# Kernel optimization log

Hardware: AMD Instinct MI355X
Metric: run time of the kernel (lower is better)

## Reference

```python
import jax, jax.numpy as jnp
import numpy as np
from jax import lax


@jax.custom_vjp
def binarize(w):
    # sign binarization of weights (XNOR-style), STE gradient in bwd
    return jnp.sign(w)

def _bin_fwd(w):
    return jnp.sign(w), w

def _bin_bwd(w, g):
    # straight-through estimator, clipped to |w| <= 1
    return (g * (jnp.abs(w) <= 1.0).astype(g.dtype),)

binarize.defvjp(_bin_fwd, _bin_bwd)


def hardtanh(x):
    return jnp.clip(x, -1.0, 1.0)


def bconv(x, w, b):
    # x: NCHW, w: OIHW, valid padding, stride 1, binarized weights
    y = lax.conv_general_dilated(
        x, binarize(w), window_strides=(1, 1), padding='VALID',
        dimension_numbers=('NCHW', 'OIHW', 'NCHW'))
    return y + b[None, :, None, None]


def maxpool2(x):
    return lax.reduce_window(x, -jnp.inf, lax.max,
                             window_dimensions=(1, 1, 2, 2),
                             window_strides=(1, 1, 2, 2),
                             padding='VALID')


def setup_inputs() -> dict:
    key = jax.random.key(0)
    ks = jax.random.split(key, 11)
    f32 = jnp.float32
    sc = 0.1  # keep weights inside the STE clip region mostly
    return {
        'x':  jax.random.normal(ks[0], (2048, 3, 32, 32), f32),
        'w1': jax.random.normal(ks[1], (100, 3, 5, 5), f32) * sc,
        'b1': jax.random.normal(ks[2], (100,), f32) * sc,
        'w2': jax.random.normal(ks[3], (16, 100, 5, 5), f32) * sc,
        'b2': jax.random.normal(ks[4], (16,), f32) * sc,
        'w3': jax.random.normal(ks[5], (120, 400), f32) * sc,
        'b3': jax.random.normal(ks[6], (120,), f32) * sc,
        'w4': jax.random.normal(ks[7], (84, 120), f32) * sc,
        'b4': jax.random.normal(ks[8], (84,), f32) * sc,
        'w5': jax.random.normal(ks[9], (10, 84), f32) * sc,
        'b5': jax.random.normal(ks[10], (10,), f32) * sc,
    }


def reference(x, w1, b1, w2, b2, w3, b3, w4, b4, w5, b5):
    h = maxpool2(hardtanh(bconv(x, w1, b1)))          # [B,100,14,14]
    h = maxpool2(hardtanh(bconv(h, w2, b2)))          # [B,16,5,5]
    h = h.reshape(h.shape[0], 16 * 5 * 5)             # [B,400]
    h = hardtanh(h @ binarize(w3).T + b3)             # [B,120]
    h = hardtanh(h @ binarize(w4).T + b4)             # [B,84]
    return h @ binarize(w5).T + b5                    # [B,10]
```

## Files before the change

kernel.cpp:

```cpp
#include <hip/hip_runtime.h>
#include <hip/hip_bf16.h>
#include <hip/hip_fp16.h>

typedef _Float16 f16x8 __attribute__((ext_vector_type(8)));
typedef float f32x4 __attribute__((ext_vector_type(4)));

union B8 { uint4 u; f16x8 h; };

__device__ __forceinline__ float htanh(float v) {
    return fminf(1.f, fmaxf(-1.f, v));
}
__device__ __forceinline__ unsigned short f2h(float f) {
    __half h = __float2half(f);
    return *reinterpret_cast<unsigned short*>(&h);
}
__device__ __forceinline__ float sxor(float h, float w) {
    return __uint_as_float(__float_as_uint(h) ^ (__float_as_uint(w) & 0x80000000u));
}

#define WSA1_OFF 102400
#define H2_OFF   138240

__global__ __launch_bounds__(256) void bn_pack(
    const float* __restrict__ w1, uint4* __restrict__ wsA1,
    const float* __restrict__ w2, uint4* __restrict__ wsA2)
{
    if (blockIdx.x < 9) {
        int t = blockIdx.x * 256 + threadIdx.x;
        if (t >= 2240) return;
        int lane = t & 63;
        int kk = (t >> 6) % 5;
        int m  = t / 320;
        int oc = m * 16 + (lane & 15), g = lane >> 4;
        unsigned int d[4];
        #pragma unroll
        for (int r = 0; r < 4; ++r) {
            int c, ky, kx; bool tv;
            if (kk < 4) { int rr = kk * 4 + g; tv = rr < 15; c = rr % 3; ky = rr / 3; kx = r; }
            else        { int s  = g * 4 + r;  tv = s  < 15; c = s  % 3; ky = s  / 3; kx = 4; }
            unsigned int v = 0u;
            if (tv && oc < 100) {
                float wv = w1[((oc * 3 + c) * 5 + ky) * 5 + kx];
                unsigned int sg = wv > 0.f ? 0x3C00u : (wv < 0.f ? 0xBC00u : 0u);
                v = sg | (sg << 16);
            }
            d[r] = v;
        }
        wsA1[t] = make_uint4(d[0], d[1], d[2], d[3]);
    } else {
        int t = (blockIdx.x - 9) * 256 + threadIdx.x;
        int lane = t & 63;
        int kk = (t >> 6) & 3;
        int s = t >> 8;
        int oc = lane & 15, g = lane >> 4;
        unsigned int d[4];
        #pragma unroll
        for (int r = 0; r < 4; ++r) {
            unsigned int u[2];
            #pragma unroll
            for (int h = 0; h < 2; ++h) {
                int ic = kk * 32 + g * 8 + r * 2 + h;
                unsigned int v = 0u;
                if (ic < 100) {
                    float wv = w2[(oc * 100 + ic) * 25 + s];
                    v = wv > 0.f ? 0x3C00u : (wv < 0.f ? 0xBC00u : 0u);
                }
                u[h] = v;
            }
            d[r] = u[0] | (u[1] << 16);
        }
        wsA2[t] = make_uint4(d[0], d[1], d[2], d[3]);
    }
}

#define HT_HALVES 29952

template<int MC>
__device__ __forceinline__ void conv1_group(
    const unsigned int* __restrict__ sxu, const uint4* __restrict__ wsA1,
    const float* b1s, unsigned short* ht, int lane, int g, int col,
    int ntStart, int mBase)
{
    f16x8 a[MC][5];
    #pragma unroll
    for (int mi = 0; mi < MC; ++mi)
        #pragma unroll
        for (int kk = 0; kk < 5; ++kk) {
            B8 t; t.u = wsA1[((mBase + mi) * 5 + kk) * 64 + lane];
            a[mi][kk] = t.h;
        }

    const int g37 = g * 37, g148 = g * 148 + 4;

    for (int nt = ntStart; nt < 13; nt += 4) {
        const int w = nt * 16 + col;
        const bool valid = w < 196;
        const int wc = valid ? w : 195;
        const int wy = wc / 14, wx = wc - wy * 14;
        const unsigned int* bt = sxu + wy * 222 + wx * 2;
        const unsigned int* b0  = bt + g37;
        const unsigned int* blx = bt + g148;

        f32x4 mx[MC];
        #pragma unroll
        for (int pass = 0; pass < 4; ++pass) {
            const int q = (pass >> 1) * 111 + (pass & 1);

            f32x4 acc[MC];
            #pragma unroll
            for (int kk = 0; kk < 5; ++kk) {
                B8 bb;
                if (kk < 4) {
                    const unsigned int* bk = b0 + kk * 148;
                    bb.u = make_uint4(bk[q], bk[q + 1], bk[q + 2], bk[q + 3]);
                } else {
                    bb.u = make_uint4(blx[q], blx[q + 37], blx[q + 74], blx[q + 111]);
                }
                #pragma unroll
                for (int mi = 0; mi < MC; ++mi) {
                    f32x4 c0 = (kk == 0) ? (f32x4){0.f, 0.f, 0.f, 0.f} : acc[mi];
                    acc[mi] = __builtin_amdgcn_mfma_f32_16x16x32_f16(a[mi][kk], bb.h, c0, 0, 0, 0);
                }
            }
            #pragma unroll
            for (int mi = 0; mi < MC; ++mi) {
                if (pass == 0) {
                    mx[mi] = acc[mi];
                } else {
                    #pragma unroll
                    for (int r = 0; r < 4; ++r)
                        mx[mi][r] = fmaxf(mx[mi][r], acc[mi][r]);
                }
            }
        }

        if (valid) {
            const int sig = wy * 18 + wx;
            #pragma unroll
            for (int mi = 0; mi < MC; ++mi) {
                const int oc0 = (mBase + mi) * 16 + g * 4;
                if (oc0 < 104) {
                    float4 bias = *(const float4*)&b1s[oc0];
                    unsigned short o0 = f2h(htanh(mx[mi][0] + bias.x));
                    unsigned short o1 = f2h(htanh(mx[mi][1] + bias.y));
                    unsigned short o2 = f2h(htanh(mx[mi][2] + bias.z));
                    unsigned short o3 = f2h(htanh(mx[mi][3] + bias.w));
                    uint2 d;
                    d.x = (unsigned int)o0 | ((unsigned int)o1 << 16);
                    d.y = (unsigned int)o2 | ((unsigned int)o3 << 16);
                    *(uint2*)(ht + sig * 120 + oc0) = d;
                }
            }
        }
    }
}

__global__ __launch_bounds__(256, 2) void bn_convs(
    const float* __restrict__ x, const uint4* __restrict__ wsA1,
    const unsigned short* __restrict__ wsA2,
    const float* __restrict__ b1, const float* __restrict__ b2,
    float* __restrict__ h2)
{
    __shared__ __align__(16) unsigned int sxu[3584];
    __shared__ __align__(16) unsigned short ht[HT_HALVES];
    __shared__ float b1s[112];
    const int img = blockIdx.x;
    const int tid = threadIdx.x;
    const int lane = tid & 63, wv = tid >> 6;

    {
        uint4* z = (uint4*)sxu;
        for (int i = tid; i < 896; i += 256) z[i] = make_uint4(0u, 0u, 0u, 0u);
        uint4* zh = (uint4*)ht;
        for (int i = tid; i < 3744; i += 256) zh[i] = make_uint4(0u, 0u, 0u, 0u);
    }
    __syncthreads();

    {
        const float4* xg = (const float4*)(x + (size_t)img * 3072);
        for (int i = tid; i < 768; i += 256) {
            float4 v = xg[i];
            float vv[4] = {v.x, v.y, v.z, v.w};
            unsigned int u[4];
            #pragma unroll
            for (int q = 0; q < 4; ++q) {
                __half h = __float2half(vv[q]);
                float rs = vv[q] - __half2float(h);
                __half rl = __float2half(rs);
                u[q] = (unsigned int)*(unsigned short*)&h |
                       ((unsigned int)*(unsigned short*)&rl << 16);
            }
            int c = i >> 8, y = (i >> 3) & 31, q4 = i & 7;
            int base = 111 * y + 37 * c + 4 * q4;
            sxu[base]     = u[0];
            sxu[base + 1] = u[1];
            sxu[base + 2] = u[2];
            sxu[base + 3] = u[3];
        }
        if (tid < 112) b1s[tid] = (tid < 100) ? b1[tid] : 0.f;
    }
    __syncthreads();

    const int g = lane >> 4;
    const int col = lane & 15;

    const int s0 = (wv + (img & 3)) & 3;
    conv1_group<4>(sxu, wsA1, b1s, ht, lane, g, col, s0, 0);
    conv1_group<3>(sxu, wsA1, b1s, ht, lane, g, col, s0, 4);
    __syncthreads();

    int bc[7];
    #pragma unroll
    for (int t = 0; t < 7; ++t) {
        int P = t * 16 + col;
        int Pc = P < 100 ? P : 99;
        bc[t] = ((Pc / 10) * 18 + (Pc % 10)) * 120 + g * 8;
    }
    f32x4 acc[7];
    #pragma unroll
    for (int t = 0; t < 7; ++t) acc[t] = (f32x4){0.f, 0.f, 0.f, 0.f};

    const f16x8* wsAv = (const f16x8*)wsA2;
    const int ko = wv * 32;
    {
        f16x8 a2[13];
        #pragma unroll
        for (int j = 0; j < 13; ++j)
            a2[j] = wsAv[((j * 4 + wv) << 6) | lane];
        #pragma unroll
        for (int s = 0; s < 13; ++s) {
            const int off = ((s / 5) * 18 + (s % 5)) * 120 + ko;
            #pragma unroll
            for (int t = 0; t < 7; ++t) {
                f16x8 bb = *(const f16x8*)&ht[bc[t] + off];
                acc[t] = __builtin_amdgcn_mfma_f32_16x16x32_f16(a2[s], bb, acc[t], 0, 0, 0);
            }
        }
    }
    {
        f16x8 a2[12];
        #pragma unroll
        for (int j = 0; j < 12; ++j)
            a2[j] = wsAv[(((13 + j) * 4 + wv) << 6) | lane];
        #pragma unroll
        for (int s = 13; s < 25; ++s) {
            const int off = ((s / 5) * 18 + (s % 5)) * 120 + ko;
            #pragma unroll
            for (int t = 0; t < 7; ++t) {
                f16x8 bb = *(const f16x8*)&ht[bc[t] + off];
                acc[t] = __builtin_amdgcn_mfma_f32_16x16x32_f16(a2[s - 13], bb, acc[t], 0, 0, 0);
            }
        }
    }
    __syncthreads();

    float* pc = (float*)ht;
    #pragma unroll
    for (int t = 0; t < 7; ++t)
        #pragma unroll
        for (int r = 0; r < 4; ++r)
            pc[(((wv * 7 + t) * 16) + (g * 4 + r)) * 16 + col] = acc[t][r];
    __syncthreads();

    float* y = (float*)ht + 7168;
    for (int i = tid; i < 1792; i += 256) {
        int t = i >> 8, rem = i & 255;
        int oc = rem >> 4, c2 = rem & 15;
        int P = t * 16 + c2;
        if (P < 100) {
            int idx = (t * 16 + oc) * 16 + c2;
            float v = pc[idx] + pc[1792 + idx] + pc[3584 + idx] + pc[5376 + idx];
            y[oc * 100 + P] = htanh(v + b2[oc]);
        }
    }
    __syncthreads();

    for (int t2 = tid; t2 < 400; t2 += 256) {
        int oc = t2 / 25, pp = t2 - oc * 25;
        int ppy = pp / 5, ppx = pp - ppy * 5;
        int base = oc * 100 + ppy * 20 + ppx * 2;
        float m = fmaxf(fmaxf(y[base], y[base + 1]),
                        fmaxf(y[base + 10], y[base + 11]));
        h2[(size_t)img * 400 + t2] = m;
    }
}

__global__ __launch_bounds__(256) void bn_fc(
    const float* __restrict__ h2,
    const float* __restrict__ w3, const float* __restrict__ b3,
    const float* __restrict__ w4, const float* __restrict__ b4,
    const float* __restrict__ w5, const float* __restrict__ b5,
    float* __restrict__ out)
{
    __shared__ float sh2[2 * 404];
    __shared__ float sh3[2 * 124];
    __shared__ float sh4[2 * 88];
    const int b0 = blockIdx.x * 2;
    const int tid = threadIdx.x;

    for (int i = tid; i < 800; i += 256) {
        int s = i / 400, k = i - s * 400;
        sh2[s * 404 + k] = h2[(size_t)(b0 + s) * 400 + k];
    }
    __syncthreads();

    for (int t = tid; t < 240; t += 256) {
        int o = t >> 1, s = t & 1;
        const float4* wr = (const float4*)(w3 + o * 400);
        const float4* hr = (const float4*)&sh2[s * 404];
        float a0 = 0.f, a1 = 0.f, a2 = 0.f, a3 = 0.f;
        #pragma unroll 5
        for (int k = 0; k < 100; ++k) {
            float4 w = wr[k], h = hr[k];
            a0 += sxor(h.x, w.x); a1 += sxor(h.y, w.y);
            a2 += sxor(h.z, w.z); a3 += sxor(h.w, w.w);
        }
        sh3[s * 124 + o] = htanh(b3[o] + ((a0 + a1) + (a2 + a3)));
    }
    __syncthreads();

    for (int t = tid; t < 168; t += 256) {
        int o = t >> 1, s = t & 1;
        const float4* wr = (const float4*)(w4 + o * 120);
        const float4* hr = (const float4*)&sh3[s * 124];
        float a0 = 0.f, a1 = 0.f, a2 = 0.f, a3 = 0.f;
        #pragma unroll
        for (int k = 0; k < 30; ++k) {
            float4 w = wr[k], h = hr[k];
            a0 += sxor(h.x, w.x); a1 += sxor(h.y, w.y);
            a2 += sxor(h.z, w.z); a3 += sxor(h.w, w.w);
        }
        sh4[s * 88 + o] = htanh(b4[o] + ((a0 + a1) + (a2 + a3)));
    }
    __syncthreads();

    for (int t = tid; t < 20; t += 256) {
        int o = t >> 1, s = t & 1;
        const float4* wr = (const float4*)(w5 + o * 84);
        const float4* hr = (const float4*)&sh4[s * 88];
        float a0 = 0.f, a1 = 0.f, a2 = 0.f, a3 = 0.f;
        #pragma unroll
        for (int k = 0; k < 21; ++k) {
            float4 w = wr[k], h = hr[k];
            a0 += sxor(h.x, w.x); a1 += sxor(h.y, w.y);
            a2 += sxor(h.z, w.z); a3 += sxor(h.w, w.w);
        }
        out[(size_t)(b0 + s) * 10 + o] = b5[o] + ((a0 + a1) + (a2 + a3));
    }
}

extern "C" void kernel_launch(void* const* d_in, const int* in_sizes, int n_in,
                              void* d_out, int out_size, void* d_ws, size_t ws_size,
                              hipStream_t stream) {
    const float* x  = (const float*)d_in[0];
    const float* w1 = (const float*)d_in[1];
    const float* b1 = (const float*)d_in[2];
    const float* w2 = (const float*)d_in[3];
    const float* b2 = (const float*)d_in[4];
    const float* w3 = (const float*)d_in[5];
    const float* b3 = (const float*)d_in[6];
    const float* w4 = (const float*)d_in[7];
    const float* b4 = (const float*)d_in[8];
    const float* w5 = (const float*)d_in[9];
    const float* b5 = (const float*)d_in[10];
    float* out = (float*)d_out;

    unsigned short* wsA2 = (unsigned short*)d_ws;
    uint4* wsA1          = (uint4*)((char*)d_ws + WSA1_OFF);
    float* h2            = (float*)((char*)d_ws + H2_OFF);

    hipLaunchKernelGGL(bn_pack, dim3(34), dim3(256), 0, stream,
                       w1, wsA1, w2, (uint4*)wsA2);
    hipLaunchKernelGGL(bn_convs, dim3(2048), dim3(256), 0, stream,
                       x, wsA1, wsA2, b1, b2, h2);
    hipLaunchKernelGGL(bn_fc, dim3(1024), dim3(256), 0, stream, h2,
                       w3, b3, w4, b4, w5, b5, out);
}
```

Baseline: 111.1 us.

## Split each image's conv stack across two blocks by output rows

The fused conv kernel now launches two blocks per image, each covering a band of output rows. Each block stages only the input rows it needs, computes the overlapping conv1 rows (a halo), and produces a subset of the pooled conv2 outputs. It also shrinks the conv1 activation tile stride from 120 to 104 halves and fuses the conv2 reduction, bias, hardtanh and maxpool into a single pass. The smaller LDS footprint is meant to raise occupancy and spread work over more blocks, at the cost of recomputing the halo conv1 rows and a dynamic inner MFMA loop that is no longer fully unrolled.

```diff
diff --git a/kernel.cpp b/kernel.cpp
--- a/kernel.cpp
+++ b/kernel.cpp
@@ -73,13 +73,14 @@
     }
 }
 
-#define HT_HALVES 29952
+#define HT_HALVES 18432
+#define SXU_WORDS 2816
 
 template<int MC>
 __device__ __forceinline__ void conv1_group(
     const unsigned int* __restrict__ sxu, const uint4* __restrict__ wsA1,
     const float* b1s, unsigned short* ht, int lane, int g, int col,
-    int ntStart, int mBase)
+    int ntStart, int mBase, int ntiles, int nwin)
 {
     f16x8 a[MC][5];
     #pragma unroll
@@ -92,11 +93,11 @@
 
     const int g37 = g * 37, g148 = g * 148 + 4;
 
-    for (int nt = ntStart; nt < 13; nt += 4) {
-        const int w = nt * 16 + col;
-        const bool valid = w < 196;
-        const int wc = valid ? w : 195;
-        const int wy = wc / 14, wx = wc - wy * 14;
+    for (int nt = ntStart; nt < ntiles; nt += 4) {
+        const int lw = nt * 16 + col;
+        const bool valid = lw < nwin;
+        const int lwc = valid ? lw : nwin - 1;
+        const int wy = lwc / 14, wx = lwc - wy * 14;
         const unsigned int* bt = sxu + wy * 222 + wx * 2;
         const unsigned int* b0  = bt + g37;
         const unsigned int* blx = bt + g148;
@@ -148,7 +149,7 @@
                     uint2 d;
                     d.x = (unsigned int)o0 | ((unsigned int)o1 << 16);
                     d.y = (unsigned int)o2 | ((unsigned int)o3 << 16);
-                    *(uint2*)(ht + sig * 120 + oc0) = d;
+                    *(uint2*)(ht + sig * 104 + oc0) = d;
                 }
             }
         }
@@ -161,25 +162,30 @@
     const float* __restrict__ b1, const float* __restrict__ b2,
     float* __restrict__ h2)
 {
-    __shared__ __align__(16) unsigned int sxu[3584];
+    __shared__ __align__(16) unsigned int sxu[SXU_WORDS];
     __shared__ __align__(16) unsigned short ht[HT_HALVES];
     __shared__ float b1s[112];
-    const int img = blockIdx.x;
+    const int img  = blockIdx.x >> 1;
+    const int half = blockIdx.x & 1;
     const int tid = threadIdx.x;
     const int lane = tid & 63, wv = tid >> 6;
 
     {
         uint4* z = (uint4*)sxu;
-        for (int i = tid; i < 896; i += 256) z[i] = make_uint4(0u, 0u, 0u, 0u);
+        for (int i = tid; i < 704; i += 256) z[i] = make_uint4(0u, 0u, 0u, 0u);
         uint4* zh = (uint4*)ht;
-        for (int i = tid; i < 3744; i += 256) zh[i] = make_uint4(0u, 0u, 0u, 0u);
+        for (int i = tid; i < 2304; i += 256) zh[i] = make_uint4(0u, 0u, 0u, 0u);
     }
     __syncthreads();
 
     {
+        const int ybase = half ? 12 : 0;
+        const int nrows = half ? 20 : 24;
         const float4* xg = (const float4*)(x + (size_t)img * 3072);
-        for (int i = tid; i < 768; i += 256) {
-            float4 v = xg[i];
+        for (int i = tid; i < nrows * 24; i += 256) {
+            int yl = i / 24, rem = i - yl * 24;
+            int c = rem >> 3, q4 = rem & 7;
+            float4 v = xg[c * 256 + (yl + ybase) * 8 + q4];
             float vv[4] = {v.x, v.y, v.z, v.w};
             unsigned int u[4];
             #pragma unroll
@@ -190,8 +196,7 @@
                 u[q] = (unsigned int)*(unsigned short*)&h |
                        ((unsigned int)*(unsigned short*)&rl << 16);
             }
-            int c = i >> 8, y = (i >> 3) & 31, q4 = i & 7;
-            int base = 111 * y + 37 * c + 4 * q4;
+            int base = 111 * yl + 37 * c + 4 * q4;
             sxu[base]     = u[0];
             sxu[base + 1] = u[1];
             sxu[base + 2] = u[2];
@@ -204,21 +209,25 @@
     const int g = lane >> 4;
     const int col = lane & 15;
 
+    const int nwin   = half ? 112 : 140;
+    const int ntiles = half ? 7 : 9;
     const int s0 = (wv + (img & 3)) & 3;
-    conv1_group<4>(sxu, wsA1, b1s, ht, lane, g, col, s0, 0);
-    conv1_group<3>(sxu, wsA1, b1s, ht, lane, g, col, s0, 4);
-    __syncthreads();
-
-    int bc[7];
+    conv1_group<4>(sxu, wsA1, b1s, ht, lane, g, col, s0, 0, ntiles, nwin);
+    conv1_group<3>(sxu, wsA1, b1s, ht, lane, g, col, s0, 4, ntiles, nwin);
+    __syncthreads();
+
+    const int NP  = half ? 40 : 60;
+    const int NT2 = half ? 3 : 4;
+    int bc[4];
     #pragma unroll
-    for (int t = 0; t < 7; ++t) {
-        int P = t * 16 + col;
-        int Pc = P < 100 ? P : 99;
-        bc[t] = ((Pc / 10) * 18 + (Pc % 10)) * 120 + g * 8;
-    }
-    f32x4 acc[7];
+    for (int ti = 0; ti < 4; ++ti) {
+        int P = ti * 16 + col;
+        int Pc = P < NP ? P : NP - 1;
+        bc[ti] = ((Pc / 10) * 18 + (Pc % 10)) * 104 + g * 8;
+    }
+    f32x4 acc[4];
     #pragma unroll
-    for (int t = 0; t < 7; ++t) acc[t] = (f32x4){0.f, 0.f, 0.f, 0.f};
+    for (int ti = 0; ti < 4; ++ti) acc[ti] = (f32x4){0.f, 0.f, 0.f, 0.f};
 
     const f16x8* wsAv = (const f16x8*)wsA2;
     const int ko = wv * 32;
@@ -229,11 +238,10 @@
             a2[j] = wsAv[((j * 4 + wv) << 6) | lane];
         #pragma unroll
         for (int s = 0; s < 13; ++s) {
-            const int off = ((s / 5) * 18 + (s % 5)) * 120 + ko;
-            #pragma unroll
-            for (int t = 0; t < 7; ++t) {
-                f16x8 bb = *(const f16x8*)&ht[bc[t] + off];
-                acc[t] = __builtin_amdgcn_mfma_f32_16x16x32_f16(a2[s], bb, acc[t], 0, 0, 0);
+            const int off = ((s / 5) * 18 + (s % 5)) * 104 + ko;
+            for (int ti = 0; ti < NT2; ++ti) {
+                f16x8 bb = *(const f16x8*)&ht[bc[ti] + off];
+                acc[ti] = __builtin_amdgcn_mfma_f32_16x16x32_f16(a2[s], bb, acc[ti], 0, 0, 0);
             }
         }
     }
@@ -244,44 +252,43 @@
             a2[j] = wsAv[(((13 + j) * 4 + wv) << 6) | lane];
         #pragma unroll
         for (int s = 13; s < 25; ++s) {
-            const int off = ((s / 5) * 18 + (s % 5)) * 120 + ko;
-            #pragma unroll
-            for (int t = 0; t < 7; ++t) {
-                f16x8 bb = *(const f16x8*)&ht[bc[t] + off];
-                acc[t] = __builtin_amdgcn_mfma_f32_16x16x32_f16(a2[s - 13], bb, acc[t], 0, 0, 0);
+            const int off = ((s / 5) * 18 + (s % 5)) * 104 + ko;
+            for (int ti = 0; ti < NT2; ++ti) {
+                f16x8 bb = *(const f16x8*)&ht[bc[ti] + off];
+                acc[ti] = __builtin_amdgcn_mfma_f32_16x16x32_f16(a2[s - 13], bb, acc[ti], 0, 0, 0);
             }
         }
     }
     __syncthreads();
 
     float* pc = (float*)ht;
-    #pragma unroll
-    for (int t = 0; t < 7; ++t)
+    for (int ti = 0; ti < NT2; ++ti)
         #pragma unroll
         for (int r = 0; r < 4; ++r)
-            pc[(((wv * 7 + t) * 16) + (g * 4 + r)) * 16 + col] = acc[t][r];
-    __syncthreads();
-
-    float* y = (float*)ht + 7168;
-    for (int i = tid; i < 1792; i += 256) {
-        int t = i >> 8, rem = i & 255;
-        int oc = rem >> 4, c2 = rem & 15;
-        int P = t * 16 + c2;
-        if (P < 100) {
-            int idx = (t * 16 + oc) * 16 + c2;
-            float v = pc[idx] + pc[1792 + idx] + pc[3584 + idx] + pc[5376 + idx];
-            y[oc * 100 + P] = htanh(v + b2[oc]);
-        }
-    }
-    __syncthreads();
-
-    for (int t2 = tid; t2 < 400; t2 += 256) {
-        int oc = t2 / 25, pp = t2 - oc * 25;
-        int ppy = pp / 5, ppx = pp - ppy * 5;
-        int base = oc * 100 + ppy * 20 + ppx * 2;
-        float m = fmaxf(fmaxf(y[base], y[base + 1]),
-                        fmaxf(y[base + 10], y[base + 11]));
-        h2[(size_t)img * 400 + t2] = m;
+            pc[((wv * 4 + ti) * 16 + (g * 4 + r)) * 16 + col] = acc[ti][r];
+    __syncthreads();
+
+    const int npp = half ? 10 : 15;
+    const int ppy_off = half ? 3 : 0;
+    const int nout = 16 * npp;
+    if (tid < nout) {
+        int oc = tid / npp, pp = tid - oc * npp;
+        int ppy_l = pp / 5, ppx = pp - ppy_l * 5;
+        float b = b2[oc];
+        float m = -3.4e38f;
+        #pragma unroll
+        for (int dy = 0; dy < 2; ++dy)
+            #pragma unroll
+            for (int dx = 0; dx < 2; ++dx) {
+                int P = (2 * ppy_l + dy) * 10 + 2 * ppx + dx;
+                int t = P >> 4, c2 = P & 15;
+                int idx = (t * 16 + oc) * 16 + c2;
+                float v = pc[idx] + pc[(64 + t * 16 + oc) * 16 + c2]
+                        + pc[(128 + t * 16 + oc) * 16 + c2]
+                        + pc[(192 + t * 16 + oc) * 16 + c2];
+                m = fmaxf(m, htanh(v + b));
+            }
+        h2[(size_t)img * 400 + oc * 25 + (ppy_off + ppy_l) * 5 + ppx] = m;
     }
 }
 
@@ -371,7 +378,7 @@
 
     hipLaunchKernelGGL(bn_pack, dim3(34), dim3(256), 0, stream,
                        w1, wsA1, w2, (uint4*)wsA2);
-    hipLaunchKernelGGL(bn_convs, dim3(2048), dim3(256), 0, stream,
+    hipLaunchKernelGGL(bn_convs, dim3(4096), dim3(256), 0, stream,
                        x, wsA1, wsA2, b1, b2, h2);
     hipLaunchKernelGGL(bn_fc, dim3(1024), dim3(256), 0, stream, h2,
                        w3, b3, w4, b4, w5, b5, out);
```

New measurement: 210.1 us. 1.89x slower.
